# Kernel tuning notes

Measured on AMD Instinct MI355X. Metric: run time of the kernel, lower is better.

## Reference

```python
import jax, jax.numpy as jnp
import numpy as np

B, T, I, H, HORIZON = 64, 512, 256, 1024, 24


def _lstm_layer(x, Wih, Whh, bih, bhh):
    """PyTorch-convention LSTM layer. x: [B,T,I_l] -> outputs [B,T,H].
    Gate order along 4H axis: i, f, g, o."""
    b = x.shape[0]
    h_dim = Whh.shape[1]
    # Precompute input contribution for all timesteps: [B,T,4H]
    xg = jnp.einsum('bti,gi->btg', x, Wih) + bih + bhh

    def step(carry, xg_t):
        h, c = carry
        gates = xg_t + h @ Whh.T  # [B,4H]
        i_g, f_g, g_g, o_g = jnp.split(gates, 4, axis=-1)
        c = jax.nn.sigmoid(f_g) * c + jax.nn.sigmoid(i_g) * jnp.tanh(g_g)
        h = jax.nn.sigmoid(o_g) * jnp.tanh(c)
        return (h, c), h

    h0 = jnp.zeros((b, h_dim), x.dtype)
    (_, _), hs = jax.lax.scan(step, (h0, h0), jnp.swapaxes(xg, 0, 1))
    return jnp.swapaxes(hs, 0, 1)  # [B,T,H]


def setup_inputs() -> dict:
    key = jax.random.key(0)
    ks = jax.random.split(key, 11)
    s_i = 1.0 / np.sqrt(H)  # PyTorch-style uniform-ish scale, use scaled normal
    return {
        'x': jax.random.normal(ks[0], (B, T, I), jnp.float32),
        'W_ih0': jax.random.normal(ks[1], (4 * H, I), jnp.float32) * s_i,
        'W_hh0': jax.random.normal(ks[2], (4 * H, H), jnp.float32) * s_i,
        'b_ih0': jax.random.normal(ks[3], (4 * H,), jnp.float32) * s_i,
        'b_hh0': jax.random.normal(ks[4], (4 * H,), jnp.float32) * s_i,
        'W_ih1': jax.random.normal(ks[5], (4 * H, H), jnp.float32) * s_i,
        'W_hh1': jax.random.normal(ks[6], (4 * H, H), jnp.float32) * s_i,
        'b_ih1': jax.random.normal(ks[7], (4 * H,), jnp.float32) * s_i,
        'b_hh1': jax.random.normal(ks[8], (4 * H,), jnp.float32) * s_i,
        'W_head': jax.random.normal(ks[9], (HORIZON, H), jnp.float32) * s_i,
        'b_head': jax.random.normal(ks[10], (HORIZON,), jnp.float32) * s_i,
    }


def reference(x, W_ih0, W_hh0, b_ih0, b_hh0, W_ih1, W_hh1, b_ih1, b_hh1, W_head, b_head):
    h1 = _lstm_layer(x, W_ih0, W_hh0, b_ih0, b_hh0)   # [B,T,H]
    h2 = _lstm_layer(h1, W_ih1, W_hh1, b_ih1, b_hh1)  # [B,T,H]
    last = h2[:, -1, :]                                # [B,H]
    return last @ W_head.T + b_head                    # [B,HORIZON]
```

## Files before the change

kernel.cpp:

```cpp
#include <hip/hip_runtime.h>


typedef _Float16 h8 __attribute__((ext_vector_type(8)));
typedef float    f4 __attribute__((ext_vector_type(4)));
typedef unsigned long long u64;

#define WS_W0P   0
#define WS_W1P   10485760
#define WS_H0Q   27262976
#define WS_H2Q   27787264
#define WS_SYNC  28049408
#define WS_XPK   28057600
#define WS_XPK_END 44834816ULL

static __device__ __forceinline__ float sigm(float v) { return 1.f / (1.f + __expf(-v)); }
static __device__ __forceinline__ float tanh_fast(float v) {
  const float e = __expf(2.f * v);
  return 1.f - 2.f / (e + 1.f);
}
static __device__ __forceinline__ h8 vload16(const _Float16* p) {
  return *(const volatile h8*)p;
}
static __device__ __forceinline__ void vstore16(_Float16* p, h8 v) {
  *(volatile h8*)p = v;
}

__global__ void prep_kernel(const float* __restrict__ x,
                            const float* __restrict__ Wih0, const float* __restrict__ Whh0,
                            const float* __restrict__ Wih1, const float* __restrict__ Whh1,
                            _Float16* __restrict__ W0p, _Float16* __restrict__ W1p,
                            _Float16* __restrict__ xpk,
                            unsigned* __restrict__ hz, unsigned* __restrict__ sync_ws)
{
  const long tid0 = (long)blockIdx.x * blockDim.x + threadIdx.x;
  const long np   = (long)gridDim.x * blockDim.x;

  for (long e = tid0; e < 5242880; e += np) {
    const int j = e & 7, quad = (e >> 3) & 3, l15 = (e >> 5) & 15, nt = (e >> 9) & 7;
    const int r = (int)(e >> 12);
    const int c = r % 40, cs = r / 40;
    const int col = nt * 16 + l15;
    const int row = (col >> 5) * 1024 + cs * 32 + (col & 31);
    const int k = c * 32 + quad * 8 + j;
    const float v = (k < 256) ? Wih0[(long)row * 256 + k] : Whh0[(long)row * 1024 + k - 256];
    W0p[e] = (_Float16)v;
  }
  for (long e = tid0; e < 8388608; e += np) {
    const int j = e & 7, quad = (e >> 3) & 3, l15 = (e >> 5) & 15, nt = (e >> 9) & 7;
    const int r = (int)(e >> 12);
    const int c = r & 63, cs = r >> 6;
    const int col = nt * 16 + l15;
    const int row = (col >> 5) * 1024 + cs * 32 + (col & 31);
    const int k = c * 32 + quad * 8 + j;
    const float v = (k < 1024) ? Wih1[(long)row * 1024 + k] : Whh1[(long)row * 1024 + k - 1024];
    W1p[e] = (_Float16)v;
  }
  if (xpk) {
    for (long e = tid0; e < 8388608; e += np) {
      const int k32 = e & 31, b16 = (e >> 5) & 15, bg = (e >> 9) & 3;
      const int c = (e >> 11) & 7;
      const int t = (int)(e >> 14);
      const int b = bg * 16 + b16, k = c * 32 + k32;
      xpk[e] = (_Float16)x[(long)b * 131072 + (long)t * 256 + k];
    }
  }
  for (long e = tid0; e < 196608; e += np) hz[e] = 0u;
  if (tid0 < 2048) sync_ws[tid0] = 0u;
}

template<bool XP>
__launch_bounds__(512, 1)
__global__ void lstm_kernel(const float* __restrict__ x, const _Float16* __restrict__ xpk,
                            const float* __restrict__ bih0, const float* __restrict__ bhh0,
                            const float* __restrict__ bih1, const float* __restrict__ bhh1,
                            const _Float16* __restrict__ W0p, const _Float16* __restrict__ W1p,
                            _Float16* __restrict__ h0q, _Float16* __restrict__ h2q,
                            unsigned* __restrict__ sy)
{
  extern __shared__ float gb[];
  __shared__ float cst[512];
  __shared__ float biasl[128];
  __shared__ _Float16 htmp[32 * 18];

  const int tid = threadIdx.x, wg = blockIdx.x;
  const int xcd = wg & 7, jdec = wg >> 3;
  const int lay = jdec & 1, jj = jdec >> 1;
  const int bg = jj & 3, csl = jj >> 2;
  const int cs = xcd * 4 + csl;
  const int lane = tid & 63, kg = tid >> 6;
  const int l15 = lane & 15, quad = lane >> 4;
  const int boff = l15 * 32 + quad * 8;
  const int aoff = bg * 512 + l15 * 32 + quad * 8;

  const _Float16* Wp = lay ? (W1p + (long)cs * 262144) : (W0p + (long)cs * 163840);

  if (tid < 128) {
    const int row = (tid >> 5) * 1024 + cs * 32 + (tid & 31);
    biasl[tid] = lay ? (bih1[row] + bhh1[row]) : (bih0[row] + bhh0[row]);
  }
  cst[tid] = 0.f;
  __syncthreads();

  unsigned* const fL0  = sy + (bg * 32);
  unsigned* const fL1  = sy + ((4 + bg) * 32);
  unsigned* const fOwn = (lay ? fL1 : fL0) + cs;

  auto spin1 = [&](const unsigned* p, int tgt) {
    while ((int)__hip_atomic_load(p, __ATOMIC_RELAXED, __HIP_MEMORY_SCOPE_AGENT) < tgt)
      __builtin_amdgcn_s_sleep(2);
  };

  const int rotd = ((l15 & 3) << 3) | (((l15 >> 2) & 1) << 2);
  auto dump = [&](const f4* acc) {
#pragma unroll
    for (int nt = 0; nt < 8; ++nt)
      *(f4*)&gb[(kg * 128 + nt * 16 + l15) * 32 + ((quad * 4 + rotd) & 31)] = acc[nt];
  };

  auto pointwise_publish = [&](_Float16* wr, int n, int gtgt) {
    __syncthreads();
    {
      const int b16 = tid & 15, hh = tid >> 4;
      const int rotr = ((hh & 3) << 3) | (((hh >> 2) & 1) << 2);
      float gv[4];
#pragma unroll
      for (int gt = 0; gt < 4; ++gt) {
        float s = biasl[gt * 32 + hh];
#pragma unroll
        for (int k = 0; k < 8; ++k)
          s += gb[(k * 128 + gt * 32 + hh) * 32 + ((b16 + rotr) & 31)];
        gv[gt] = s;
      }
      const float si = sigm(gv[0]), sf = sigm(gv[1]);
      const float tg = tanh_fast(gv[2]), so = sigm(gv[3]);
      const float cn = sf * cst[tid] + si * tg;
      cst[tid] = cn;
      htmp[hh * 18 + b16] = (_Float16)(so * tanh_fast(cn));
    }
    __syncthreads();
    if (tid < 64) {
      if (tid < 32) spin1(fL1 + tid, gtgt);
      const int b16 = tid & 15, q = tid >> 4;
      union { h8 v; _Float16 e[8]; } r;
#pragma unroll
      for (int i = 0; i < 8; ++i) r.e[i] = htmp[(q * 8 + i) * 18 + b16];
      vstore16(wr + (cs * 4 + bg) * 512 + b16 * 32 + q * 8, r.v);
      asm volatile("s_waitcnt vmcnt(0)" ::: "memory");
      if (tid == 0)
        __hip_atomic_store(fOwn, (unsigned)(n + 1),
                           __ATOMIC_RELAXED, __HIP_MEMORY_SCOPE_AGENT);
    }
  };

  if (lay == 0) {
    const int c0 = kg * 5;
    for (int n = 0; n < 512; ++n) {
      const _Float16* h0prev = h0q + ((n - 1) & 3) * 65536;
      const _Float16* xs = XP ? (xpk + (long)n * 16384) : nullptr;

      f4 acc[8] = {};
      h8 Ab[5]; h8 Bb[2][8];
      auto loadB = [&](int c, int sl) {
        const _Float16* bp = Wp + (long)c * 4096 + boff;
#pragma unroll
        for (int nt = 0; nt < 8; ++nt) Bb[sl][nt] = *(const h8*)(bp + nt * 512);
      };
      auto loadA = [&](int c, int idx) {
        if (c < 8) {
          if (XP) Ab[idx] = *(const h8*)(xs + c * 2048 + aoff);
          else {
            const float* q = x + (long)(bg * 16 + l15) * 131072 + (long)n * 256 + c * 32 + quad * 8;
            const f4 v0 = *(const f4*)q;
            const f4 v1 = *(const f4*)(q + 4);
            h8 t;
            t[0]=(_Float16)v0[0]; t[1]=(_Float16)v0[1]; t[2]=(_Float16)v0[2]; t[3]=(_Float16)v0[3];
            t[4]=(_Float16)v1[0]; t[5]=(_Float16)v1[1]; t[6]=(_Float16)v1[2]; t[7]=(_Float16)v1[3];
            Ab[idx] = t;
          }
        } else {
          Ab[idx] = vload16(h0prev + (c - 8) * 2048 + aoff);
        }
      };

      loadB(c0, 0);
#pragma unroll
      for (int i = 0; i < 5; ++i)
        if (c0 + i < 8) loadA(c0 + i, i);

      if (lane < 5) {
        const int c = c0 + lane;
        if (c >= 8) spin1(fL0 + (c - 8), n);
      }

#pragma unroll
      for (int i = 0; i < 5; ++i)
        if (c0 + i >= 8) loadA(c0 + i, i);

#pragma unroll
      for (int i = 0; i < 5; ++i) {
        if (i + 1 < 5) loadB(c0 + i + 1, (i + 1) & 1);
        const h8 A = Ab[i];
#pragma unroll
        for (int nt = 0; nt < 8; ++nt)
          acc[nt] = __builtin_amdgcn_mfma_f32_16x16x32_f16(A, Bb[i & 1][nt], acc[nt], 0, 0, 0);
      }
      dump(acc);
      pointwise_publish(h0q + (n & 3) * 65536, n, n - 3);
    }
  } else {
    const int c0 = kg * 4;
    for (int n = 0; n < 512; ++n) {
      const _Float16* h0cur  = h0q + (n & 3) * 65536;
      const _Float16* h2prev = h2q + ((n - 1) & 1) * 65536;

      f4 acc[8] = {};
      h8 Ab[4]; h8 Bb[2][8];
      auto loadB = [&](int c, int sl) {
        const _Float16* bp = Wp + (long)c * 4096 + boff;
#pragma unroll
        for (int nt = 0; nt < 8; ++nt) Bb[sl][nt] = *(const h8*)(bp + nt * 512);
      };
      auto loadA = [&](const _Float16* hb, int cloc, int idx) {
        Ab[idx] = vload16(hb + cloc * 2048 + aoff);
      };

      loadB(c0, 0);
      if (lane < 4) spin1(fL0 + c0 + lane, n + 1);
#pragma unroll
      for (int i = 0; i < 4; ++i) loadA(h0cur, c0 + i, i);
#pragma unroll
      for (int i = 0; i < 4; ++i) {
        if (i + 1 < 4) loadB(c0 + i + 1, (i + 1) & 1);
        const h8 A = Ab[i];
#pragma unroll
        for (int nt = 0; nt < 8; ++nt)
          acc[nt] = __builtin_amdgcn_mfma_f32_16x16x32_f16(A, Bb[i & 1][nt], acc[nt], 0, 0, 0);
      }

      loadB(32 + c0, 0);
      if (lane < 4) spin1(fL1 + c0 + lane, n);
#pragma unroll
      for (int i = 0; i < 4; ++i) loadA(h2prev, c0 + i, i);
#pragma unroll
      for (int i = 0; i < 4; ++i) {
        if (i + 1 < 4) loadB(32 + c0 + i + 1, (i + 1) & 1);
        const h8 A = Ab[i];
#pragma unroll
        for (int nt = 0; nt < 8; ++nt)
          acc[nt] = __builtin_amdgcn_mfma_f32_16x16x32_f16(A, Bb[i & 1][nt], acc[nt], 0, 0, 0);
      }
      dump(acc);
      pointwise_publish(h2q + (n & 1) * 65536, n, n);
    }
  }
}

__global__ void head_kernel(const _Float16* __restrict__ h2s, const float* __restrict__ Wh,
                            const float* __restrict__ bh, float* __restrict__ out)
{
  const int blk = blockIdx.x;
  const int b = blk / 24, j = blk % 24;
  const int lane = threadIdx.x;
  float sum = 0.f;
#pragma unroll
  for (int k0 = 0; k0 < 1024; k0 += 64) {
    const int hid = k0 + lane;
    const float hv = (float)h2s[((hid >> 5) * 4 + (b >> 4)) * 512 + (b & 15) * 32 + (hid & 31)];
    sum += hv * Wh[(long)j * 1024 + hid];
  }
#pragma unroll
  for (int off = 32; off > 0; off >>= 1)
    sum += __shfl_down(sum, off, 64);
  if (lane == 0) out[b * 24 + j] = sum + bh[j];
}

extern "C" void kernel_launch(void* const* d_in, const int* in_sizes, int n_in,
                              void* d_out, int out_size, void* d_ws, size_t ws_size,
                              hipStream_t stream)
{
  const float* x    = (const float*)d_in[0];
  const float* Wih0 = (const float*)d_in[1];
  const float* Whh0 = (const float*)d_in[2];
  const float* bih0 = (const float*)d_in[3];
  const float* bhh0 = (const float*)d_in[4];
  const float* Wih1 = (const float*)d_in[5];
  const float* Whh1 = (const float*)d_in[6];
  const float* bih1 = (const float*)d_in[7];
  const float* bhh1 = (const float*)d_in[8];
  const float* Whd  = (const float*)d_in[9];
  const float* bhd  = (const float*)d_in[10];

  char* ws = (char*)d_ws;
  _Float16* W0p     = (_Float16*)(ws + WS_W0P);
  _Float16* W1p     = (_Float16*)(ws + WS_W1P);
  _Float16* h0q     = (_Float16*)(ws + WS_H0Q);
  _Float16* h2q     = (_Float16*)(ws + WS_H2Q);
  unsigned* sync_ws = (unsigned*)(ws + WS_SYNC);
  float* out = (float*)d_out;

  const bool use_xpk = (ws_size >= WS_XPK_END);
  _Float16* xpk = use_xpk ? (_Float16*)(ws + WS_XPK) : nullptr;

  prep_kernel<<<dim3(2048), dim3(256), 0, stream>>>(
      x, Wih0, Whh0, Wih1, Whh1, W0p, W1p, xpk,
      (unsigned*)(ws + WS_H0Q), sync_ws);

  if (use_xpk)
    lstm_kernel<true><<<dim3(256), dim3(512), 131072, stream>>>(
        x, xpk, bih0, bhh0, bih1, bhh1, W0p, W1p, h0q, h2q, sync_ws);
  else
    lstm_kernel<false><<<dim3(256), dim3(512), 131072, stream>>>(
        x, nullptr, bih0, bhh0, bih1, bhh1, W0p, W1p, h0q, h2q, sync_ws);

  head_kernel<<<dim3(64 * 24), dim3(64), 0, stream>>>(
      h2q + 65536, Whd, bhd, out);
}
```

Baseline: 4.551 ms.

## Cache spin-flag values and reorder layer-1 recurrent loads before input loads

```diff
diff --git a/kernel.cpp b/kernel.cpp
--- a/kernel.cpp
+++ b/kernel.cpp
@@ -105,10 +105,13 @@
   unsigned* const fL1  = sy + ((4 + bg) * 32);
   unsigned* const fOwn = (lay ? fL1 : fL0) + cs;
 
-  auto spin1 = [&](const unsigned* p, int tgt) {
-    while ((int)__hip_atomic_load(p, __ATOMIC_RELAXED, __HIP_MEMORY_SCOPE_AGENT) < tgt)
-      __builtin_amdgcn_s_sleep(2);
+  auto spinc = [&](const unsigned* p, int tgt, int& cache) {
+    while (cache < tgt) {
+      cache = (int)__hip_atomic_load(p, __ATOMIC_RELAXED, __HIP_MEMORY_SCOPE_AGENT);
+      if (cache < tgt) __builtin_amdgcn_s_sleep(2);
+    }
   };
+  int cGate = 0;
 
   const int rotd = ((l15 & 3) << 3) | (((l15 >> 2) & 1) << 2);
   auto dump = [&](const f4* acc) {
@@ -117,7 +120,7 @@
       *(f4*)&gb[(kg * 128 + nt * 16 + l15) * 32 + ((quad * 4 + rotd) & 31)] = acc[nt];
   };
 
-  auto pointwise_publish = [&](_Float16* wr, int n, int gtgt) {
+  auto pointwise_publish = [&](_Float16* wr, int n, int gtgt, bool gated) {
     __syncthreads();
     {
       const int b16 = tid & 15, hh = tid >> 4;
@@ -139,7 +142,7 @@
     }
     __syncthreads();
     if (tid < 64) {
-      if (tid < 32) spin1(fL1 + tid, gtgt);
+      if (gated && tid < 32) spinc(fL1 + tid, gtgt, cGate);
       const int b16 = tid & 15, q = tid >> 4;
       union { h8 v; _Float16 e[8]; } r;
 #pragma unroll
@@ -154,6 +157,7 @@
 
   if (lay == 0) {
     const int c0 = kg * 5;
+    int cSelf = 0;
     for (int n = 0; n < 512; ++n) {
       const _Float16* h0prev = h0q + ((n - 1) & 3) * 65536;
       const _Float16* xs = XP ? (xpk + (long)n * 16384) : nullptr;
@@ -189,7 +193,7 @@
 
       if (lane < 5) {
         const int c = c0 + lane;
-        if (c >= 8) spin1(fL0 + (c - 8), n);
+        if (c >= 8) spinc(fL0 + (c - 8), n, cSelf);
       }
 
 #pragma unroll
@@ -205,52 +209,53 @@
           acc[nt] = __builtin_amdgcn_mfma_f32_16x16x32_f16(A, Bb[i & 1][nt], acc[nt], 0, 0, 0);
       }
       dump(acc);
-      pointwise_publish(h0q + (n & 3) * 65536, n, n - 3);
+      pointwise_publish(h0q + (n & 3) * 65536, n, n - 3, true);
     }
   } else {
     const int c0 = kg * 4;
+    int cA = 0;
+    int cB = 0;
     for (int n = 0; n < 512; ++n) {
       const _Float16* h0cur  = h0q + (n & 3) * 65536;
       const _Float16* h2prev = h2q + ((n - 1) & 1) * 65536;
 
       f4 acc[8] = {};
-      h8 Ab[4]; h8 Bb[2][8];
+      h8 Ab[4]; h8 Cb[4]; h8 Bb[2][8];
       auto loadB = [&](int c, int sl) {
         const _Float16* bp = Wp + (long)c * 4096 + boff;
 #pragma unroll
         for (int nt = 0; nt < 8; ++nt) Bb[sl][nt] = *(const h8*)(bp + nt * 512);
       };
-      auto loadA = [&](const _Float16* hb, int cloc, int idx) {
-        Ab[idx] = vload16(hb + cloc * 2048 + aoff);
+
+      if (lane < 4) spinc(fL0 + c0 + lane, n + 1, cA);
+      Ab[0] = vload16(h0cur + (c0 + 0) * 2048 + aoff);
+      Ab[1] = vload16(h0cur + (c0 + 1) * 2048 + aoff);
+      Ab[2] = vload16(h0cur + (c0 + 2) * 2048 + aoff);
+      Ab[3] = vload16(h0cur + (c0 + 3) * 2048 + aoff);
+      loadB(32 + c0, 0);
+      loadB(32 + c0 + 1, 1);
+
+      if (lane < 4) spinc(fL1 + c0 + lane, n, cB);
+      Cb[0] = vload16(h2prev + (c0 + 0) * 2048 + aoff);
+      Cb[1] = vload16(h2prev + (c0 + 1) * 2048 + aoff);
+      Cb[2] = vload16(h2prev + (c0 + 2) * 2048 + aoff);
+      Cb[3] = vload16(h2prev + (c0 + 3) * 2048 + aoff);
+
+      auto mfma8 = [&](const h8 A, const h8* B) {
+#pragma unroll
+        for (int nt = 0; nt < 8; ++nt)
+          acc[nt] = __builtin_amdgcn_mfma_f32_16x16x32_f16(A, B[nt], acc[nt], 0, 0, 0);
       };
-
-      loadB(c0, 0);
-      if (lane < 4) spin1(fL0 + c0 + lane, n + 1);
-#pragma unroll
-      for (int i = 0; i < 4; ++i) loadA(h0cur, c0 + i, i);
-#pragma unroll
-      for (int i = 0; i < 4; ++i) {
-        if (i + 1 < 4) loadB(c0 + i + 1, (i + 1) & 1);
-        const h8 A = Ab[i];
-#pragma unroll
-        for (int nt = 0; nt < 8; ++nt)
-          acc[nt] = __builtin_amdgcn_mfma_f32_16x16x32_f16(A, Bb[i & 1][nt], acc[nt], 0, 0, 0);
-      }
-
-      loadB(32 + c0, 0);
-      if (lane < 4) spin1(fL1 + c0 + lane, n);
-#pragma unroll
-      for (int i = 0; i < 4; ++i) loadA(h2prev, c0 + i, i);
-#pragma unroll
-      for (int i = 0; i < 4; ++i) {
-        if (i + 1 < 4) loadB(32 + c0 + i + 1, (i + 1) & 1);
-        const h8 A = Ab[i];
-#pragma unroll
-        for (int nt = 0; nt < 8; ++nt)
-          acc[nt] = __builtin_amdgcn_mfma_f32_16x16x32_f16(A, Bb[i & 1][nt], acc[nt], 0, 0, 0);
-      }
+      mfma8(Cb[0], Bb[0]); loadB(32 + c0 + 2, 0);
+      mfma8(Cb[1], Bb[1]); loadB(32 + c0 + 3, 1);
+      mfma8(Cb[2], Bb[0]); loadB(c0, 0);
+      mfma8(Cb[3], Bb[1]); loadB(c0 + 1, 1);
+      mfma8(Ab[0], Bb[0]); loadB(c0 + 2, 0);
+      mfma8(Ab[1], Bb[1]); loadB(c0 + 3, 1);
+      mfma8(Ab[2], Bb[0]);
+      mfma8(Ab[3], Bb[1]);
       dump(acc);
-      pointwise_publish(h2q + (n & 1) * 65536, n, n);
+      pointwise_publish(h2q + (n & 1) * 65536, n, 0, false);
     }
   }
 }
```

Measured after the change: 5.267 ms. 15.8% more time.

## Replace per-step flag spinning with in-band sentinel polling on hidden-state buffers

Applied to the files above, without the earlier changes.

```diff
diff --git a/kernel.cpp b/kernel.cpp
--- a/kernel.cpp
+++ b/kernel.cpp
@@ -3,15 +3,14 @@
 
 typedef _Float16 h8 __attribute__((ext_vector_type(8)));
 typedef float    f4 __attribute__((ext_vector_type(4)));
-typedef unsigned long long u64;
 
 #define WS_W0P   0
 #define WS_W1P   10485760
 #define WS_H0Q   27262976
-#define WS_H2Q   27787264
-#define WS_SYNC  28049408
-#define WS_XPK   28057600
-#define WS_XPK_END 44834816ULL
+#define WS_H2Q   28311552
+#define WS_SYNC  28835840
+#define WS_XPK   28844032
+#define WS_XPK_END 45621248ULL
 
 static __device__ __forceinline__ float sigm(float v) { return 1.f / (1.f + __expf(-v)); }
 static __device__ __forceinline__ float tanh_fast(float v) {
@@ -64,7 +63,12 @@
       xpk[e] = (_Float16)x[(long)b * 131072 + (long)t * 256 + k];
     }
   }
-  for (long e = tid0; e < 196608; e += np) hz[e] = 0u;
+  for (long e = tid0; e < 393216; e += np) {
+    unsigned v;
+    if (e < 262144) v = ((e >> 15) == 7) ? 0u : 0x7C007C00u;
+    else            v = (((e - 262144) >> 15) == 3) ? 0u : 0x7C007C00u;
+    hz[e] = v;
+  }
   if (tid0 < 2048) sync_ws[tid0] = 0u;
 }
 
@@ -101,14 +105,9 @@
   cst[tid] = 0.f;
   __syncthreads();
 
-  unsigned* const fL0  = sy + (bg * 32);
   unsigned* const fL1  = sy + ((4 + bg) * 32);
-  unsigned* const fOwn = (lay ? fL1 : fL0) + cs;
-
-  auto spin1 = [&](const unsigned* p, int tgt) {
-    while ((int)__hip_atomic_load(p, __ATOMIC_RELAXED, __HIP_MEMORY_SCOPE_AGENT) < tgt)
-      __builtin_amdgcn_s_sleep(2);
-  };
+  unsigned* const fOwn = fL1 + cs;
+  int gateCache = 0;
 
   const int rotd = ((l15 & 3) << 3) | (((l15 >> 2) & 1) << 2);
   auto dump = [&](const f4* acc) {
@@ -117,7 +116,7 @@
       *(f4*)&gb[(kg * 128 + nt * 16 + l15) * 32 + ((quad * 4 + rotd) & 31)] = acc[nt];
   };
 
-  auto pointwise_publish = [&](_Float16* wr, int n, int gtgt) {
+  auto pointwise_publish = [&](_Float16* wr, _Float16* pz, int n) {
     __syncthreads();
     {
       const int b16 = tid & 15, hh = tid >> 4;
@@ -139,14 +138,25 @@
     }
     __syncthreads();
     if (tid < 64) {
-      if (tid < 32) spin1(fL1 + tid, gtgt);
+      if (lay == 0 && tid < 32) {
+        const int tgt = n - 3;
+        while (gateCache < tgt) {
+          gateCache = (int)__hip_atomic_load(fL1 + tid, __ATOMIC_RELAXED,
+                                             __HIP_MEMORY_SCOPE_AGENT);
+          if (gateCache < tgt) __builtin_amdgcn_s_sleep(2);
+        }
+      }
       const int b16 = tid & 15, q = tid >> 4;
+      const int off = (cs * 4 + bg) * 512 + b16 * 32 + q * 8;
       union { h8 v; _Float16 e[8]; } r;
 #pragma unroll
       for (int i = 0; i < 8; ++i) r.e[i] = htmp[(q * 8 + i) * 18 + b16];
-      vstore16(wr + (cs * 4 + bg) * 512 + b16 * 32 + q * 8, r.v);
-      asm volatile("s_waitcnt vmcnt(0)" ::: "memory");
-      if (tid == 0)
+      vstore16(wr + off, r.v);
+      union { h8 v; unsigned short u[8]; } P;
+#pragma unroll
+      for (int i = 0; i < 8; ++i) P.u[i] = 0x7C00;
+      vstore16(pz + off, P.v);
+      if (lay == 1 && tid == 0)
         __hip_atomic_store(fOwn, (unsigned)(n + 1),
                            __ATOMIC_RELAXED, __HIP_MEMORY_SCOPE_AGENT);
     }
@@ -155,7 +165,7 @@
   if (lay == 0) {
     const int c0 = kg * 5;
     for (int n = 0; n < 512; ++n) {
-      const _Float16* h0prev = h0q + ((n - 1) & 3) * 65536;
+      const _Float16* h0prev = h0q + ((n - 1) & 7) * 65536;
       const _Float16* xs = XP ? (xpk + (long)n * 16384) : nullptr;
 
       f4 acc[8] = {};
@@ -165,36 +175,38 @@
 #pragma unroll
         for (int nt = 0; nt < 8; ++nt) Bb[sl][nt] = *(const h8*)(bp + nt * 512);
       };
-      auto loadA = [&](int c, int idx) {
-        if (c < 8) {
-          if (XP) Ab[idx] = *(const h8*)(xs + c * 2048 + aoff);
-          else {
-            const float* q = x + (long)(bg * 16 + l15) * 131072 + (long)n * 256 + c * 32 + quad * 8;
-            const f4 v0 = *(const f4*)q;
-            const f4 v1 = *(const f4*)(q + 4);
-            h8 t;
-            t[0]=(_Float16)v0[0]; t[1]=(_Float16)v0[1]; t[2]=(_Float16)v0[2]; t[3]=(_Float16)v0[3];
-            t[4]=(_Float16)v1[0]; t[5]=(_Float16)v1[1]; t[6]=(_Float16)v1[2]; t[7]=(_Float16)v1[3];
-            Ab[idx] = t;
+      auto loadAx = [&](int c, int idx) {
+        if (XP) Ab[idx] = *(const h8*)(xs + c * 2048 + aoff);
+        else {
+          const float* q = x + (long)(bg * 16 + l15) * 131072 + (long)n * 256 + c * 32 + quad * 8;
+          const f4 v0 = *(const f4*)q;
+          const f4 v1 = *(const f4*)(q + 4);
+          h8 t;
+          t[0]=(_Float16)v0[0]; t[1]=(_Float16)v0[1]; t[2]=(_Float16)v0[2]; t[3]=(_Float16)v0[3];
+          t[4]=(_Float16)v1[0]; t[5]=(_Float16)v1[1]; t[6]=(_Float16)v1[2]; t[7]=(_Float16)v1[3];
+          Ab[idx] = t;
+        }
+      };
+
+      loadB(c0, 0);
+#pragma unroll
+      for (int i = 0; i < 5; ++i)
+        if (c0 + i < 8) loadAx(c0 + i, i);
+
+      {
+        union U { h8 v; unsigned short u[8]; };
+        for (;;) {
+          bool ok = true;
+#pragma unroll
+          for (int i = 0; i < 5; ++i) if (c0 + i >= 8) {
+            U t; t.v = vload16(h0prev + (c0 + i - 8) * 2048 + aoff);
+            Ab[i] = t.v;
+            ok = ok && (t.u[7] != 0x7C00);
           }
-        } else {
-          Ab[idx] = vload16(h0prev + (c - 8) * 2048 + aoff);
-        }
-      };
-
-      loadB(c0, 0);
-#pragma unroll
-      for (int i = 0; i < 5; ++i)
-        if (c0 + i < 8) loadA(c0 + i, i);
-
-      if (lane < 5) {
-        const int c = c0 + lane;
-        if (c >= 8) spin1(fL0 + (c - 8), n);
-      }
-
-#pragma unroll
-      for (int i = 0; i < 5; ++i)
-        if (c0 + i >= 8) loadA(c0 + i, i);
+          if (ok) break;
+          __builtin_amdgcn_s_sleep(1);
+        }
+      }
 
 #pragma unroll
       for (int i = 0; i < 5; ++i) {
@@ -205,13 +217,14 @@
           acc[nt] = __builtin_amdgcn_mfma_f32_16x16x32_f16(A, Bb[i & 1][nt], acc[nt], 0, 0, 0);
       }
       dump(acc);
-      pointwise_publish(h0q + (n & 3) * 65536, n, n - 3);
+      pointwise_publish(h0q + (n & 7) * 65536,
+                        h0q + ((n + 4) & 7) * 65536, n);
     }
   } else {
     const int c0 = kg * 4;
     for (int n = 0; n < 512; ++n) {
-      const _Float16* h0cur  = h0q + (n & 3) * 65536;
-      const _Float16* h2prev = h2q + ((n - 1) & 1) * 65536;
+      const _Float16* h0cur  = h0q + (n & 7) * 65536;
+      const _Float16* h2prev = h2q + ((n - 1) & 3) * 65536;
 
       f4 acc[8] = {};
       h8 Ab[4]; h8 Bb[2][8];
@@ -220,14 +233,22 @@
 #pragma unroll
         for (int nt = 0; nt < 8; ++nt) Bb[sl][nt] = *(const h8*)(bp + nt * 512);
       };
-      auto loadA = [&](const _Float16* hb, int cloc, int idx) {
-        Ab[idx] = vload16(hb + cloc * 2048 + aoff);
-      };
 
       loadB(c0, 0);
-      if (lane < 4) spin1(fL0 + c0 + lane, n + 1);
-#pragma unroll
-      for (int i = 0; i < 4; ++i) loadA(h0cur, c0 + i, i);
+      {
+        union U { h8 v; unsigned short u[8]; };
+        for (;;) {
+          bool ok = true;
+#pragma unroll
+          for (int i = 0; i < 4; ++i) {
+            U t; t.v = vload16(h0cur + (c0 + i) * 2048 + aoff);
+            Ab[i] = t.v;
+            ok = ok && (t.u[7] != 0x7C00);
+          }
+          if (ok) break;
+          __builtin_amdgcn_s_sleep(1);
+        }
+      }
 #pragma unroll
       for (int i = 0; i < 4; ++i) {
         if (i + 1 < 4) loadB(c0 + i + 1, (i + 1) & 1);
@@ -238,9 +259,20 @@
       }
 
       loadB(32 + c0, 0);
-      if (lane < 4) spin1(fL1 + c0 + lane, n);
-#pragma unroll
-      for (int i = 0; i < 4; ++i) loadA(h2prev, c0 + i, i);
+      {
+        union U { h8 v; unsigned short u[8]; };
+        for (;;) {
+          bool ok = true;
+#pragma unroll
+          for (int i = 0; i < 4; ++i) {
+            U t; t.v = vload16(h2prev + (c0 + i) * 2048 + aoff);
+            Ab[i] = t.v;
+            ok = ok && (t.u[7] != 0x7C00);
+          }
+          if (ok) break;
+          __builtin_amdgcn_s_sleep(1);
+        }
+      }
 #pragma unroll
       for (int i = 0; i < 4; ++i) {
         if (i + 1 < 4) loadB(32 + c0 + i + 1, (i + 1) & 1);
@@ -250,7 +282,8 @@
           acc[nt] = __builtin_amdgcn_mfma_f32_16x16x32_f16(A, Bb[i & 1][nt], acc[nt], 0, 0, 0);
       }
       dump(acc);
-      pointwise_publish(h2q + (n & 1) * 65536, n, n);
+      pointwise_publish(h2q + (n & 3) * 65536,
+                        h2q + ((n + 2) & 3) * 65536, n);
     }
   }
 }
@@ -313,5 +346,5 @@
         x, nullptr, bih0, bhh0, bih1, bhh1, W0p, W1p, h0q, h2q, sync_ws);
 
   head_kernel<<<dim3(64 * 24), dim3(64), 0, stream>>>(
-      h2q + 65536, Whd, bhd, out);
-}
+      h2q + 3 * 65536, Whd, bhd, out);
+}
```

Measured after the change: 4.875 ms. +7.1%, slower.
